# Kernel optimization log

Measured on AMD Instinct MI355X. Metric: run time of the kernel, lower is better.

The kernel has to match this reference:

```python
import jax, jax.numpy as jnp
import numpy as np

B, T, S, D, H, DK = 2, 2048, 2048, 1024, 16, 64


def setup_inputs() -> dict:
    key = jax.random.key(0)
    ks = jax.random.split(key, 11)
    s = 1.0 / np.sqrt(D)
    return {
        "query": jax.random.normal(ks[0], (B, T, D), jnp.float32),
        "value": jax.random.normal(ks[1], (B, S, D), jnp.float32),
        "key": jax.random.normal(ks[2], (B, S, D), jnp.float32),
        "Wq": jax.random.normal(ks[3], (D, H, DK), jnp.float32) * s,
        "bq": jnp.zeros((H, DK), jnp.float32),
        "Wk": jax.random.normal(ks[4], (D, H, DK), jnp.float32) * s,
        "bk": jnp.zeros((H, DK), jnp.float32),
        "Wv": jax.random.normal(ks[5], (D, H, DK), jnp.float32) * s,
        "bv": jnp.zeros((H, DK), jnp.float32),
        "Wo": jax.random.normal(ks[6], (H, DK, D), jnp.float32) * (1.0 / np.sqrt(H * DK)),
        "bo": jnp.zeros((D,), jnp.float32),
    }


def reference(query, value, key, Wq, bq, Wk, bk, Wv, bv, Wo, bo):
    # Projections: (B, seq, D) x (D, H, DK) -> (B, seq, H, DK)
    q = jnp.einsum("btd,dhk->bthk", query, Wq) + bq
    k = jnp.einsum("bsd,dhk->bshk", key, Wk) + bk
    v = jnp.einsum("bsd,dhk->bshk", value, Wv) + bv
    # Scaled dot-product attention (keras scales query by 1/sqrt(key_dim))
    q = q * (1.0 / np.sqrt(DK)).astype(np.float32)
    scores = jnp.einsum("bshk,bthk->bhts", k, q)  # (B, H, T, S)
    probs = jax.nn.softmax(scores, axis=-1)
    attn = jnp.einsum("bhts,bshk->bthk", probs, v)  # (B, T, H, DK)
    # Output projection back to model dim
    out = jnp.einsum("bthk,hkd->btd", attn, Wo) + bo
    return out
```

## Files before the change

### kernel.cpp

```cpp
#include <hip/hip_runtime.h>
#include <math.h>

#define BB  2
#define TT  2048
#define SSQ 2048
#define DD  1024
#define HH  16
#define DKK 64
#define MM  (BB*TT)
#define NN  (HH*DKK)

typedef __attribute__((ext_vector_type(8))) short short8;
typedef __attribute__((ext_vector_type(4))) float f32x4;

__device__ __forceinline__ short f2bf(float x) {
    unsigned u = __builtin_bit_cast(unsigned, x);
    unsigned r = (u + 0x7FFFu + ((u >> 16) & 1u)) >> 16;
    return (short)r;
}

__device__ __forceinline__ void glds16(const void* g, void* l) {
    __builtin_amdgcn_global_load_lds(
        (const __attribute__((address_space(1))) void*)g,
        (__attribute__((address_space(3))) void*)l, 16, 0, 0);
}

__global__ __launch_bounds__(256)
void to_bf16_acts(const float* __restrict__ a0, const float* __restrict__ a1,
                  const float* __restrict__ a2,
                  short* __restrict__ o0, short* __restrict__ o1,
                  short* __restrict__ o2)
{
    int z = blockIdx.y;
    const float* in = (z == 0) ? a0 : (z == 1) ? a1 : a2;
    short* out = (z == 0) ? o0 : (z == 1) ? o1 : o2;
    size_t i0 = ((size_t)blockIdx.x * 256 + threadIdx.x) * 8;
    f32x4 f0 = *(const f32x4*)(in + i0);
    f32x4 f1 = *(const f32x4*)(in + i0 + 4);
    short8 v;
#pragma unroll
    for (int j = 0; j < 4; j++) v[j] = f2bf(f0[j]);
#pragma unroll
    for (int j = 0; j < 4; j++) v[4 + j] = f2bf(f1[j]);
    *(short8*)(out + i0) = v;
}

__global__ __launch_bounds__(256)
void wtrans(const float* __restrict__ w0, const float* __restrict__ w1,
            const float* __restrict__ w2, const float* __restrict__ w3,
            short* __restrict__ t0, short* __restrict__ t1,
            short* __restrict__ t2, short* __restrict__ t3)
{
    __shared__ float Ls[64][65];
    int z = blockIdx.z;
    const float* in = (z == 0) ? w0 : (z == 1) ? w1 : (z == 2) ? w2 : w3;
    short* out = (z == 0) ? t0 : (z == 1) ? t1 : (z == 2) ? t2 : t3;
    const int r0 = blockIdx.y * 64, c0 = blockIdx.x * 64;
    const int t = threadIdx.x;
    const int r = t >> 2, c4 = t & 3;

    const float* src = in + (size_t)(r0 + r) * DD + c0 + c4 * 16;
#pragma unroll
    for (int i = 0; i < 4; i++) {
        f32x4 f = *(const f32x4*)(src + i * 4);
#pragma unroll
        for (int j = 0; j < 4; j++) Ls[r][c4 * 16 + i * 4 + j] = f[j];
    }
    __syncthreads();

    short8 va, vb;
#pragma unroll
    for (int j = 0; j < 8; j++) va[j] = f2bf(Ls[c4 * 16 + j][r]);
#pragma unroll
    for (int j = 0; j < 8; j++) vb[j] = f2bf(Ls[c4 * 16 + 8 + j][r]);
    short* dst = out + (size_t)(c0 + r) * DD + r0 + c4 * 16;
    *(short8*)dst = va;
    *(short8*)(dst + 8) = vb;
}

__device__ __forceinline__ void gemm_core(const short* __restrict__ A,
                                          const short* __restrict__ Bt,
                                          int m0, int n0,
                                          short* As, short* Bs,
                                          f32x4 (&acc)[4][4])
{
    const int tid = threadIdx.x;
    const int w = tid >> 6, l = tid & 63;
    const int l15 = l & 15, quad = l >> 4;
    const int wm = w >> 1, wn = w & 1;

#pragma unroll
    for (int i = 0; i < 4; i++)
#pragma unroll
        for (int j = 0; j < 4; j++) acc[i][j] = (f32x4){0.f, 0.f, 0.f, 0.f};

    const int r = tid >> 2, cseg = tid & 3;
    const short* gA = A + (size_t)(m0 + r) * DD + cseg * 8;
    const short* gB = Bt + (size_t)(n0 + r) * DD + cseg * 8;
    short* ldsA = As + w * 512;
    short* ldsB = Bs + w * 512;

    for (int k0 = 0; k0 < DD; k0 += 32) {
        glds16(gA + k0,                 ldsA);
        glds16(gA + (size_t)64 * DD + k0, ldsA + 2048);
        glds16(gB + k0,                 ldsB);
        glds16(gB + (size_t)64 * DD + k0, ldsB + 2048);
        __syncthreads();

        short8 bF[4];
#pragma unroll
        for (int ni = 0; ni < 4; ni++)
            bF[ni] = *(const short8*)&Bs[(wn * 64 + ni * 16 + l15) * 32 + quad * 8];
#pragma unroll
        for (int mi = 0; mi < 4; mi++) {
            short8 aF = *(const short8*)&As[(wm * 64 + mi * 16 + l15) * 32 + quad * 8];
#pragma unroll
            for (int ni = 0; ni < 4; ni++)
                acc[mi][ni] = __builtin_amdgcn_mfma_f32_16x16x32_bf16(aF, bF[ni], acc[mi][ni], 0, 0, 0);
        }
        __syncthreads();
    }
}

__global__ __launch_bounds__(256, 3)
void gemm_qkv(const short* __restrict__ Aq, const short* __restrict__ Ak,
              const short* __restrict__ Av,
              const short* __restrict__ Wqt, const short* __restrict__ Wkt,
              const short* __restrict__ Wvt,
              const float* __restrict__ bq, const float* __restrict__ bk,
              const float* __restrict__ bv,
              short* __restrict__ Qb, short* __restrict__ Kb,
              short* __restrict__ Vbt)
{
    __shared__ short As[128 * 32];
    __shared__ short Bs[128 * 32];
    const int z = blockIdx.z;
    const short* A  = (z == 0) ? Aq : (z == 1) ? Ak : Av;
    const short* Bt = (z == 0) ? Wqt : (z == 1) ? Wkt : Wvt;
    const float* bias = (z == 0) ? bq : (z == 1) ? bk : bv;
    const int m0 = blockIdx.y * 128, n0 = blockIdx.x * 128;

    f32x4 acc[4][4];
    gemm_core(A, Bt, m0, n0, As, Bs, acc);

    const int tid = threadIdx.x;
    const int w = tid >> 6, l = tid & 63;
    const int l15 = l & 15, quad = l >> 4;
    const int wm = w >> 1, wn = w & 1;
    const float scale = (z == 0) ? 0.1803368801f : 1.0f;

#pragma unroll
    for (int mi = 0; mi < 4; mi++) {
#pragma unroll
        for (int reg = 0; reg < 4; reg++) {
            int m = m0 + wm * 64 + mi * 16 + quad * 4 + reg;
            int b = m >> 11, t = m & 2047;
#pragma unroll
            for (int ni = 0; ni < 4; ni++) {
                int n = n0 + wn * 64 + ni * 16 + l15;
                float vv = (acc[mi][ni][reg] + bias[n]) * scale;
                short s16 = f2bf(vv);
                int h = n >> 6, dk = n & 63;
                if (z < 2) {
                    short* dst = (z == 0) ? Qb : Kb;
                    dst[((size_t)(b * HH + h) * TT + t) * DKK + dk] = s16;
                } else {
                    Vbt[((size_t)(b * HH + h) * DKK + dk) * SSQ + t] = s16;
                }
            }
        }
    }
}

__global__ __launch_bounds__(256, 3)
void gemm_out(const short* __restrict__ Ab, const short* __restrict__ Wot,
              const float* __restrict__ bo, float* __restrict__ out)
{
    __shared__ short As[128 * 32];
    __shared__ short Bs[128 * 32];
    const int m0 = blockIdx.y * 128, n0 = blockIdx.x * 128;

    f32x4 acc[4][4];
    gemm_core(Ab, Wot, m0, n0, As, Bs, acc);

    const int tid = threadIdx.x;
    const int w = tid >> 6, l = tid & 63;
    const int l15 = l & 15, quad = l >> 4;
    const int wm = w >> 1, wn = w & 1;

#pragma unroll
    for (int mi = 0; mi < 4; mi++) {
#pragma unroll
        for (int reg = 0; reg < 4; reg++) {
            int m = m0 + wm * 64 + mi * 16 + quad * 4 + reg;
#pragma unroll
            for (int ni = 0; ni < 4; ni++) {
                int n = n0 + wn * 64 + ni * 16 + l15;
                out[(size_t)m * DD + n] = acc[mi][ni][reg] + bo[n];
            }
        }
    }
}

__global__ __launch_bounds__(256, 4)
void attn_mfma(const short* __restrict__ Qb, const short* __restrict__ Kb,
               const short* __restrict__ Vbt, short* __restrict__ Ab)
{
    __shared__ short QPs[64 * 72];
    __shared__ short Ks[64 * 72];
    __shared__ short Vs[64 * 72];

    const int tid = threadIdx.x;
    const int w = tid >> 6, l = tid & 63;
    const int l15 = l & 15, quad = l >> 4;
    const int bh = blockIdx.y;
    const int t0 = blockIdx.x * 64;
    const size_t hb = (size_t)bh * SSQ * DKK;
    const int r = tid >> 2, c4 = tid & 3;

    {
        const short* g = Qb + hb + (size_t)(t0 + r) * 64 + c4 * 16;
        short* s = QPs + r * 72 + c4 * 16;
        *(short8*)(s + 0) = *(const short8*)(g + 0);
        *(short8*)(s + 8) = *(const short8*)(g + 8);
    }
    __threadfence_block();
    short8 qf[2];
    qf[0] = *(const short8*)&QPs[(16 * w + l15) * 72 + quad * 8];
    qf[1] = *(const short8*)&QPs[(16 * w + l15) * 72 + 32 + quad * 8];

    const short* gkb = Kb + hb + (size_t)r * 64 + c4 * 16;
    const short* gvb = Vbt + hb + (size_t)r * SSQ + c4 * 16;
    short8 kr0 = *(const short8*)(gkb + 0);
    short8 kr1 = *(const short8*)(gkb + 8);
    short8 vr0 = *(const short8*)(gvb + 0);
    short8 vr1 = *(const short8*)(gvb + 8);

    f32x4 o[4];
#pragma unroll
    for (int j = 0; j < 4; j++) o[j] = (f32x4){0.f, 0.f, 0.f, 0.f};
    float lsum[4] = {0.f, 0.f, 0.f, 0.f};

    short* sk = Ks + r * 72 + c4 * 16;
    short* sv = Vs + r * 72 + c4 * 16;

    for (int s0 = 0; s0 < SSQ; s0 += 64) {
        __syncthreads();
        *(short8*)(sk + 0) = kr0;
        *(short8*)(sk + 8) = kr1;
        *(short8*)(sv + 0) = vr0;
        *(short8*)(sv + 8) = vr1;
        if (s0 + 64 < SSQ) {
            const short* gk = gkb + (size_t)(s0 + 64) * 64;
            const short* gv = gvb + (s0 + 64);
            kr0 = *(const short8*)(gk + 0);
            kr1 = *(const short8*)(gk + 8);
            vr0 = *(const short8*)(gv + 0);
            vr1 = *(const short8*)(gv + 8);
        }
        __syncthreads();

        f32x4 sc[4];
#pragma unroll
        for (int j = 0; j < 4; j++) sc[j] = (f32x4){0.f, 0.f, 0.f, 0.f};
#pragma unroll
        for (int kk = 0; kk < 2; kk++) {
#pragma unroll
            for (int np = 0; np < 4; np++) {
                short8 bK = *(const short8*)&Ks[(16 * np + l15) * 72 + kk * 32 + quad * 8];
                sc[np] = __builtin_amdgcn_mfma_f32_16x16x32_bf16(qf[kk], bK, sc[np], 0, 0, 0);
            }
        }

        {
            int prow = (16 * w + quad * 4) * 72 + l15;
#pragma unroll
            for (int reg = 0; reg < 4; reg++) {
                int pr = prow + reg * 72;
#pragma unroll
                for (int np = 0; np < 4; np++) {
                    float p = __builtin_amdgcn_exp2f(sc[np][reg]);
                    QPs[pr + 16 * np] = (short)(__builtin_bit_cast(unsigned, p) >> 16);
                    lsum[reg] += p;
                }
            }
        }
        __threadfence_block();

#pragma unroll
        for (int kk = 0; kk < 2; kk++) {
            short8 aP = *(const short8*)&QPs[(16 * w + l15) * 72 + kk * 32 + quad * 8];
#pragma unroll
            for (int np = 0; np < 4; np++) {
                short8 bV = *(const short8*)&Vs[(16 * np + l15) * 72 + kk * 32 + quad * 8];
                o[np] = __builtin_amdgcn_mfma_f32_16x16x32_bf16(aP, bV, o[np], 0, 0, 0);
            }
        }
    }

    const int b = bh >> 4, h = bh & 15;
#pragma unroll
    for (int reg = 0; reg < 4; reg++) {
        float ls = lsum[reg];
        ls += __shfl_xor(ls, 1);
        ls += __shfl_xor(ls, 2);
        ls += __shfl_xor(ls, 4);
        ls += __shfl_xor(ls, 8);
        float inv = 1.f / ls;
        int t = t0 + 16 * w + quad * 4 + reg;
#pragma unroll
        for (int np = 0; np < 4; np++) {
            Ab[((size_t)(b * TT + t) * HH + h) * DKK + 16 * np + l15] =
                f2bf(o[np][reg] * inv);
        }
    }
}

extern "C" void kernel_launch(void* const* d_in, const int* in_sizes, int n_in,
                              void* d_out, int out_size, void* d_ws, size_t ws_size,
                              hipStream_t stream)
{
    const float* query = (const float*)d_in[0];
    const float* value = (const float*)d_in[1];
    const float* key   = (const float*)d_in[2];
    const float* Wq    = (const float*)d_in[3];
    const float* bq    = (const float*)d_in[4];
    const float* Wk    = (const float*)d_in[5];
    const float* bk    = (const float*)d_in[6];
    const float* Wv    = (const float*)d_in[7];
    const float* bv    = (const float*)d_in[8];
    const float* Wo    = (const float*)d_in[9];
    const float* bo    = (const float*)d_in[10];
    float* out = (float*)d_out;

    const size_t actE = (size_t)MM * DD;
    const size_t wE   = (size_t)DD * NN;
    short* p = (short*)d_ws;
    short* Aq  = p; p += actE;
    short* Ak  = p; p += actE;
    short* Av  = p; p += actE;
    short* Wqt = p; p += wE;
    short* Wkt = p; p += wE;
    short* Wvt = p; p += wE;
    short* Wot = p; p += wE;
    short* Qb  = p; p += actE;
    short* Kb  = p; p += actE;
    short* Vbt = p; p += actE;
    short* Ab  = p; p += actE;

    dim3 blk(256);

    to_bf16_acts<<<dim3((unsigned)(actE / 2048), 3), blk, 0, stream>>>(
        query, key, value, Aq, Ak, Av);

    wtrans<<<dim3(16, 16, 4), blk, 0, stream>>>(Wq, Wk, Wv, Wo, Wqt, Wkt, Wvt, Wot);

    gemm_qkv<<<dim3(NN / 128, MM / 128, 3), blk, 0, stream>>>(
        Aq, Ak, Av, Wqt, Wkt, Wvt, bq, bk, bv, Qb, Kb, Vbt);

    attn_mfma<<<dim3(TT / 64, BB * HH), blk, 0, stream>>>(Qb, Kb, Vbt, Ab);

    gemm_out<<<dim3(DD / 128, MM / 128), blk, 0, stream>>>(Ab, Wot, bo, out);
}
```

Measured before the change: 253.8 us.

## Double attention query tile per block and add separate V transpose kernel

The attention kernel now processes 128 query rows per block (two 16-row MFMA fragments per wave), so each K/V tile loaded into shared memory serves twice as many rows. The grid is halved and occupancy hint lowered to 2. Separately, the QKV GEMM epilogue now writes V in the same row-major layout as Q/K, avoiding the strided transposed scatter, and a new vtrans kernel transposes V through shared memory. This adds an extra launch and an extra pass over V in exchange for coalesced stores and better K/V reuse.

```diff
diff --git a/kernel.cpp b/kernel.cpp
--- a/kernel.cpp
+++ b/kernel.cpp
@@ -78,6 +78,30 @@
     *(short8*)(dst + 8) = vb;
 }
 
+__global__ __launch_bounds__(256)
+void vtrans(const short* __restrict__ in, short* __restrict__ out)
+{
+    __shared__ short Ls[64][72];
+    const int bh = blockIdx.y;
+    const int t0 = blockIdx.x * 64;
+    const int tid = threadIdx.x;
+    const int r = tid >> 2, c4 = tid & 3;
+
+    const short* src = in + ((size_t)bh * TT + t0 + r) * DKK + c4 * 16;
+    *(short8*)&Ls[r][c4 * 16]     = *(const short8*)(src);
+    *(short8*)&Ls[r][c4 * 16 + 8] = *(const short8*)(src + 8);
+    __syncthreads();
+
+    short8 a, b;
+#pragma unroll
+    for (int j = 0; j < 8; j++) a[j] = Ls[c4 * 16 + j][r];
+#pragma unroll
+    for (int j = 0; j < 8; j++) b[j] = Ls[c4 * 16 + 8 + j][r];
+    short* dst = out + ((size_t)bh * DKK + r) * SSQ + t0 + c4 * 16;
+    *(short8*)dst = a;
+    *(short8*)(dst + 8) = b;
+}
+
 __device__ __forceinline__ void gemm_core(const short* __restrict__ A,
                                           const short* __restrict__ Bt,
                                           int m0, int n0,
@@ -130,7 +154,7 @@
               const float* __restrict__ bq, const float* __restrict__ bk,
               const float* __restrict__ bv,
               short* __restrict__ Qb, short* __restrict__ Kb,
-              short* __restrict__ Vbt)
+              short* __restrict__ Vtmp)
 {
     __shared__ short As[128 * 32];
     __shared__ short Bs[128 * 32];
@@ -138,6 +162,7 @@
     const short* A  = (z == 0) ? Aq : (z == 1) ? Ak : Av;
     const short* Bt = (z == 0) ? Wqt : (z == 1) ? Wkt : Wvt;
     const float* bias = (z == 0) ? bq : (z == 1) ? bk : bv;
+    short* dst = (z == 0) ? Qb : (z == 1) ? Kb : Vtmp;
     const int m0 = blockIdx.y * 128, n0 = blockIdx.x * 128;
 
     f32x4 acc[4][4];
@@ -159,14 +184,8 @@
             for (int ni = 0; ni < 4; ni++) {
                 int n = n0 + wn * 64 + ni * 16 + l15;
                 float vv = (acc[mi][ni][reg] + bias[n]) * scale;
-                short s16 = f2bf(vv);
                 int h = n >> 6, dk = n & 63;
-                if (z < 2) {
-                    short* dst = (z == 0) ? Qb : Kb;
-                    dst[((size_t)(b * HH + h) * TT + t) * DKK + dk] = s16;
-                } else {
-                    Vbt[((size_t)(b * HH + h) * DKK + dk) * SSQ + t] = s16;
-                }
+                dst[((size_t)(b * HH + h) * TT + t) * DKK + dk] = f2bf(vv);
             }
         }
     }
@@ -202,11 +221,11 @@
     }
 }
 
-__global__ __launch_bounds__(256, 4)
+__global__ __launch_bounds__(256, 2)
 void attn_mfma(const short* __restrict__ Qb, const short* __restrict__ Kb,
                const short* __restrict__ Vbt, short* __restrict__ Ab)
 {
-    __shared__ short QPs[64 * 72];
+    __shared__ short QPs[128 * 72];
     __shared__ short Ks[64 * 72];
     __shared__ short Vs[64 * 72];
 
@@ -214,20 +233,26 @@
     const int w = tid >> 6, l = tid & 63;
     const int l15 = l & 15, quad = l >> 4;
     const int bh = blockIdx.y;
-    const int t0 = blockIdx.x * 64;
+    const int t0 = blockIdx.x * 128;
     const size_t hb = (size_t)bh * SSQ * DKK;
     const int r = tid >> 2, c4 = tid & 3;
 
     {
-        const short* g = Qb + hb + (size_t)(t0 + r) * 64 + c4 * 16;
-        short* s = QPs + r * 72 + c4 * 16;
-        *(short8*)(s + 0) = *(const short8*)(g + 0);
-        *(short8*)(s + 8) = *(const short8*)(g + 8);
+        int r2 = tid >> 1, half = tid & 1;
+        const short* g = Qb + hb + (size_t)(t0 + r2) * 64 + half * 32;
+        short* s = QPs + r2 * 72 + half * 32;
+        *(short8*)(s + 0)  = *(const short8*)(g + 0);
+        *(short8*)(s + 8)  = *(const short8*)(g + 8);
+        *(short8*)(s + 16) = *(const short8*)(g + 16);
+        *(short8*)(s + 24) = *(const short8*)(g + 24);
     }
     __threadfence_block();
-    short8 qf[2];
-    qf[0] = *(const short8*)&QPs[(16 * w + l15) * 72 + quad * 8];
-    qf[1] = *(const short8*)&QPs[(16 * w + l15) * 72 + 32 + quad * 8];
+    short8 qf[2][2];
+#pragma unroll
+    for (int mf = 0; mf < 2; mf++)
+#pragma unroll
+        for (int kk = 0; kk < 2; kk++)
+            qf[mf][kk] = *(const short8*)&QPs[(32 * w + 16 * mf + l15) * 72 + kk * 32 + quad * 8];
 
     const short* gkb = Kb + hb + (size_t)r * 64 + c4 * 16;
     const short* gvb = Vbt + hb + (size_t)r * SSQ + c4 * 16;
@@ -236,10 +261,16 @@
     short8 vr0 = *(const short8*)(gvb + 0);
     short8 vr1 = *(const short8*)(gvb + 8);
 
-    f32x4 o[4];
-#pragma unroll
-    for (int j = 0; j < 4; j++) o[j] = (f32x4){0.f, 0.f, 0.f, 0.f};
-    float lsum[4] = {0.f, 0.f, 0.f, 0.f};
+    f32x4 o[2][4];
+#pragma unroll
+    for (int mf = 0; mf < 2; mf++)
+#pragma unroll
+        for (int j = 0; j < 4; j++) o[mf][j] = (f32x4){0.f, 0.f, 0.f, 0.f};
+    float lsum[2][4];
+#pragma unroll
+    for (int mf = 0; mf < 2; mf++)
+#pragma unroll
+        for (int j = 0; j < 4; j++) lsum[mf][j] = 0.f;
 
     short* sk = Ks + r * 72 + c4 * 16;
     short* sv = Vs + r * 72 + c4 * 16;
@@ -260,28 +291,32 @@
         }
         __syncthreads();
 
-        f32x4 sc[4];
-#pragma unroll
-        for (int j = 0; j < 4; j++) sc[j] = (f32x4){0.f, 0.f, 0.f, 0.f};
+        f32x4 sc[2][4];
+#pragma unroll
+        for (int mf = 0; mf < 2; mf++)
+#pragma unroll
+            for (int j = 0; j < 4; j++) sc[mf][j] = (f32x4){0.f, 0.f, 0.f, 0.f};
 #pragma unroll
         for (int kk = 0; kk < 2; kk++) {
 #pragma unroll
             for (int np = 0; np < 4; np++) {
                 short8 bK = *(const short8*)&Ks[(16 * np + l15) * 72 + kk * 32 + quad * 8];
-                sc[np] = __builtin_amdgcn_mfma_f32_16x16x32_bf16(qf[kk], bK, sc[np], 0, 0, 0);
-            }
-        }
-
-        {
-            int prow = (16 * w + quad * 4) * 72 + l15;
+                sc[0][np] = __builtin_amdgcn_mfma_f32_16x16x32_bf16(qf[0][kk], bK, sc[0][np], 0, 0, 0);
+                sc[1][np] = __builtin_amdgcn_mfma_f32_16x16x32_bf16(qf[1][kk], bK, sc[1][np], 0, 0, 0);
+            }
+        }
+
+#pragma unroll
+        for (int mf = 0; mf < 2; mf++) {
+            int prow = (32 * w + 16 * mf + quad * 4) * 72 + l15;
 #pragma unroll
             for (int reg = 0; reg < 4; reg++) {
                 int pr = prow + reg * 72;
 #pragma unroll
                 for (int np = 0; np < 4; np++) {
-                    float p = __builtin_amdgcn_exp2f(sc[np][reg]);
+                    float p = __builtin_amdgcn_exp2f(sc[mf][np][reg]);
                     QPs[pr + 16 * np] = (short)(__builtin_bit_cast(unsigned, p) >> 16);
-                    lsum[reg] += p;
+                    lsum[mf][reg] += p;
                 }
             }
         }
@@ -289,29 +324,34 @@
 
 #pragma unroll
         for (int kk = 0; kk < 2; kk++) {
-            short8 aP = *(const short8*)&QPs[(16 * w + l15) * 72 + kk * 32 + quad * 8];
+            short8 aP0 = *(const short8*)&QPs[(32 * w + l15) * 72 + kk * 32 + quad * 8];
+            short8 aP1 = *(const short8*)&QPs[(32 * w + 16 + l15) * 72 + kk * 32 + quad * 8];
 #pragma unroll
             for (int np = 0; np < 4; np++) {
                 short8 bV = *(const short8*)&Vs[(16 * np + l15) * 72 + kk * 32 + quad * 8];
-                o[np] = __builtin_amdgcn_mfma_f32_16x16x32_bf16(aP, bV, o[np], 0, 0, 0);
+                o[0][np] = __builtin_amdgcn_mfma_f32_16x16x32_bf16(aP0, bV, o[0][np], 0, 0, 0);
+                o[1][np] = __builtin_amdgcn_mfma_f32_16x16x32_bf16(aP1, bV, o[1][np], 0, 0, 0);
             }
         }
     }
 
     const int b = bh >> 4, h = bh & 15;
 #pragma unroll
-    for (int reg = 0; reg < 4; reg++) {
-        float ls = lsum[reg];
-        ls += __shfl_xor(ls, 1);
-        ls += __shfl_xor(ls, 2);
-        ls += __shfl_xor(ls, 4);
-        ls += __shfl_xor(ls, 8);
-        float inv = 1.f / ls;
-        int t = t0 + 16 * w + quad * 4 + reg;
-#pragma unroll
-        for (int np = 0; np < 4; np++) {
-            Ab[((size_t)(b * TT + t) * HH + h) * DKK + 16 * np + l15] =
-                f2bf(o[np][reg] * inv);
+    for (int mf = 0; mf < 2; mf++) {
+#pragma unroll
+        for (int reg = 0; reg < 4; reg++) {
+            float ls = lsum[mf][reg];
+            ls += __shfl_xor(ls, 1);
+            ls += __shfl_xor(ls, 2);
+            ls += __shfl_xor(ls, 4);
+            ls += __shfl_xor(ls, 8);
+            float inv = 1.f / ls;
+            int t = t0 + 32 * w + 16 * mf + quad * 4 + reg;
+#pragma unroll
+            for (int np = 0; np < 4; np++) {
+                Ab[((size_t)(b * TT + t) * HH + h) * DKK + 16 * np + l15] =
+                    f2bf(o[mf][np][reg] * inv);
+            }
         }
     }
 }
@@ -336,17 +376,18 @@
     const size_t actE = (size_t)MM * DD;
     const size_t wE   = (size_t)DD * NN;
     short* p = (short*)d_ws;
-    short* Aq  = p; p += actE;
-    short* Ak  = p; p += actE;
-    short* Av  = p; p += actE;
-    short* Wqt = p; p += wE;
-    short* Wkt = p; p += wE;
-    short* Wvt = p; p += wE;
-    short* Wot = p; p += wE;
-    short* Qb  = p; p += actE;
-    short* Kb  = p; p += actE;
-    short* Vbt = p; p += actE;
-    short* Ab  = p; p += actE;
+    short* Aq   = p; p += actE;
+    short* Ak   = p; p += actE;
+    short* Av   = p; p += actE;
+    short* Wqt  = p; p += wE;
+    short* Wkt  = p; p += wE;
+    short* Wvt  = p; p += wE;
+    short* Wot  = p; p += wE;
+    short* Qb   = p; p += actE;
+    short* Kb   = p; p += actE;
+    short* Vtmp = p; p += actE;
+    short* Vbt  = p; p += actE;
+    short* Ab   = p; p += actE;
 
     dim3 blk(256);
 
@@ -356,9 +397,11 @@
     wtrans<<<dim3(16, 16, 4), blk, 0, stream>>>(Wq, Wk, Wv, Wo, Wqt, Wkt, Wvt, Wot);
 
     gemm_qkv<<<dim3(NN / 128, MM / 128, 3), blk, 0, stream>>>(
-        Aq, Ak, Av, Wqt, Wkt, Wvt, bq, bk, bv, Qb, Kb, Vbt);
-
-    attn_mfma<<<dim3(TT / 64, BB * HH), blk, 0, stream>>>(Qb, Kb, Vbt, Ab);
+        Aq, Ak, Av, Wqt, Wkt, Wvt, bq, bk, bv, Qb, Kb, Vtmp);
+
+    vtrans<<<dim3(TT / 64, BB * HH), blk, 0, stream>>>(Vtmp, Vbt);
+
+    attn_mfma<<<dim3(TT / 128, BB * HH), blk, 0, stream>>>(Qb, Kb, Vbt, Ab);
 
     gemm_out<<<dim3(DD / 128, MM / 128), blk, 0, stream>>>(Ab, Wot, bo, out);
 }
```

Result: faster. 240.9 us (-5.1%).
